# Optimization experiments

Hardware: AMD Instinct MI355X
Metric: run time of the kernel (lower is better)

## Reference

```python
import jax, jax.numpy as jnp
import numpy as np

DIM, E, K = 256, 8, 2
B, D, H, W = 1, 32, 32, 32
EPS = 1e-5


def setup_inputs() -> dict:
    key = jax.random.key(0)
    ks = jax.random.split(key, 16)
    nrm = lambda k, s, sc=0.02: jax.random.normal(k, s, jnp.float32) * sc
    def resblock_params(k):
        k1, k2, k3, k4 = jax.random.split(k, 4)
        return dict(
            c1w=nrm(k1, (DIM, DIM, 3, 3, 3)), c1b=jnp.zeros((DIM,), jnp.float32),
            g1=jax.random.uniform(k2, (DIM,), jnp.float32, 0.5, 1.5), be1=jnp.zeros((DIM,), jnp.float32),
            c2w=nrm(k3, (DIM, DIM, 3, 3, 3)), c2b=jnp.zeros((DIM,), jnp.float32),
            g2=jax.random.uniform(k4, (DIM,), jnp.float32, 0.5, 1.5), be2=jnp.zeros((DIM,), jnp.float32),
        )
    p1 = resblock_params(ks[5])
    p2 = resblock_params(ks[6])
    return {
        "x": jax.random.normal(ks[0], (B, DIM, D, H, W), jnp.float32),
        "wg": nrm(ks[1], (DIM, E)),
        "w1": nrm(ks[2], (E, DIM, DIM)), "b1": jnp.zeros((E, DIM), jnp.float32),
        "w2": nrm(ks[3], (E, DIM, DIM)), "b2": jnp.zeros((E, DIM), jnp.float32),
        "r1_c1w": p1["c1w"], "r1_c1b": p1["c1b"], "r1_g1": p1["g1"], "r1_be1": p1["be1"],
        "r1_c2w": p1["c2w"], "r1_c2b": p1["c2b"], "r1_g2": p1["g2"], "r1_be2": p1["be2"],
        "r2_c1w": p2["c1w"], "r2_c1b": p2["c1b"], "r2_g1": p2["g1"], "r2_be1": p2["be1"],
        "r2_c2w": p2["c2w"], "r2_c2b": p2["c2b"], "r2_g2": p2["g2"], "r2_be2": p2["be2"],
        "c8w": nrm(ks[4], (DIM, DIM, 1, 1, 1)), "c8b": jnp.zeros((DIM,), jnp.float32),
    }


def conv3d(x, w, b, pad):
    y = jax.lax.conv_general_dilated(
        x, w, window_strides=(1, 1, 1), padding=[(pad, pad)] * 3,
        dimension_numbers=("NCDHW", "OIDHW", "NCDHW"))
    return y + b[None, :, None, None, None]


def batchnorm(x, g, b):
    m = x.mean(axis=(0, 2, 3, 4), keepdims=True)
    v = x.var(axis=(0, 2, 3, 4), keepdims=True)
    return g[None, :, None, None, None] * (x - m) * jax.lax.rsqrt(v + EPS) + b[None, :, None, None, None]


def unet_res_block(x, c1w, c1b, g1, be1, c2w, c2b, g2, be2):
    out = jax.nn.leaky_relu(batchnorm(conv3d(x, c1w, c1b, 1), g1, be1), 0.01)
    out = batchnorm(conv3d(out, c2w, c2b, 1), g2, be2)
    return jax.nn.leaky_relu(out + x, 0.01)  # identity shortcut (in==out ch, stride 1)


def mom_block(x, wg, w1, b1, w2, b2):
    Bb, C, Dd, Hh, Ww = x.shape
    tokens = x.transpose(0, 2, 3, 4, 1).reshape(-1, C)  # [T, C]
    T = tokens.shape[0]
    probs = jax.nn.softmax(tokens @ wg, axis=-1)          # [T, E]
    vals, idx = jax.lax.top_k(probs, K)                   # [T, K]
    wts = vals / vals.sum(-1, keepdims=True)
    gates = jnp.zeros((T, E), probs.dtype).at[jnp.arange(T)[:, None], idx].set(wts)
    # dense expert MLPs (math-equivalent to gather/dispatch/combine)
    h = jax.nn.gelu(jnp.einsum("tc,ech->eth", tokens, w1) + b1[:, None, :])
    eo = jnp.einsum("eth,ehc->etc", h, w2) + b2[:, None, :]
    moe = jnp.einsum("te,etc->tc", gates, eo)             # [T, C]
    # switch-style load-balancing auxiliary loss
    density = (gates > 0).astype(probs.dtype).mean(0)     # fraction of tokens per expert
    density_proxy = probs.mean(0)
    aux = (density * density_proxy).sum() * E
    out = x + moe.reshape(Bb, Dd, Hh, Ww, C).transpose(0, 4, 1, 2, 3)
    return out, aux


def reference(x, wg, w1, b1, w2, b2,
              r1_c1w, r1_c1b, r1_g1, r1_be1, r1_c2w, r1_c2b, r1_g2, r1_be2,
              r2_c1w, r2_c1b, r2_g1, r2_be1, r2_c2w, r2_c2b, r2_g2, r2_be2,
              c8w, c8b):
    xm, aux = mom_block(x, wg, w1, b1, w2, b2)
    res = unet_res_block(xm, r1_c1w, r1_c1b, r1_g1, r1_be1, r1_c2w, r1_c2b, r1_g2, r1_be2)
    res = unet_res_block(res, r2_c1w, r2_c1b, r2_g1, r2_be1, r2_c2w, r2_c2b, r2_g2, r2_be2)
    out = xm + conv3d(res, c8w, c8b, 0)  # Dropout3d is identity at eval
    return out, aux
```

## Files before the change

kernel.cpp:

```cpp
#include <hip/hip_runtime.h>
#include <stdint.h>

typedef __attribute__((ext_vector_type(8))) short short8;
typedef __attribute__((ext_vector_type(4))) float f32x4;
typedef unsigned short u16;
typedef unsigned int u32;
typedef unsigned long long u64;

#define WS_TOK   0ull
#define WS_XT    16777216ull
#define WS_XMCT  50331648ull
#define WS_GATES 83886080ull
#define WS_H     84934656ull
#define WS_P1    135266304ull
#define WS_P2    155389952ull
#define WS_Y     175513600ull
#define WS_R2    209068032ull
#define WS_WRB   225845248ull
#define WS_W1P   240001024ull
#define WS_W2P   241049600ull
#define WS_C8P   242098176ull
#define WS_PART  242229248ull
#define WS_SF    243277824ull
#define WS_AUXP  243279872ull

#define WS_PERM  (WS_H + 0x00000ull)
#define WS_TBL   (WS_H + 0x60000ull)
#define WS_META  (WS_H + 0x70000ull)
#define WS_BCNT  (WS_H + 0x80000ull)
#define WS_BOFF  (WS_H + 0x90000ull)
#define WS_SEL   (WS_H + 0x100000ull)

__device__ __forceinline__ u16 f2bf(float f) {
  u32 x = __float_as_uint(f);
  u32 r = x + 0x7fffu + ((x >> 16) & 1u);
  return (u16)(r >> 16);
}
__device__ __forceinline__ float bf2f(u32 u) { return __uint_as_float(u << 16); }

__global__ void trans_in_k(const float* __restrict__ x, float* __restrict__ xt,
                           u16* __restrict__ tok) {
  __shared__ float ld[64][65];
  int tt = blockIdx.x, cc = blockIdx.y, tid = threadIdx.x;
#pragma unroll
  for (int k = 0; k < 16; ++k) {
    int idx = tid + k * 256;
    int cl = idx >> 6, j = idx & 63;
    ld[cl][j] = x[(size_t)(cc * 64 + cl) * 32768 + tt * 64 + j];
  }
  __syncthreads();
#pragma unroll
  for (int k = 0; k < 16; ++k) {
    int idx = tid + k * 256;
    int tl = idx >> 6, cl = idx & 63;
    float v = ld[cl][tl];
    size_t o = (size_t)(tt * 64 + tl) * 256 + cc * 64 + cl;
    xt[o] = v;
    tok[o] = f2bf(v);
  }
}

__global__ void pack_rb_k(const float* __restrict__ w0, const float* __restrict__ w1,
                          const float* __restrict__ w2, const float* __restrict__ w3,
                          u16* __restrict__ out) {
  __shared__ float ld[6912];
  int conv = blockIdx.x >> 8, blk = blockIdx.x & 255, tid = threadIdx.x;
  const float* src = conv == 0 ? w0 : conv == 1 ? w1 : conv == 2 ? w2 : w3;
  size_t base = (size_t)blk * 256 * 27;
#pragma unroll
  for (int k = 0; k < 27; ++k) ld[tid + k * 256] = src[base + tid + k * 256];
  __syncthreads();
  u16* dst = out + (size_t)conv * 27 * 65536;
  int n = blk * 256 + tid;
#pragma unroll
  for (int tap = 0; tap < 27; ++tap)
    dst[(size_t)tap * 65536 + n] = f2bf(ld[tid * 27 + tap]);
}

__global__ void pack_tr_k(const float* __restrict__ w1, const float* __restrict__ w2,
                          u16* __restrict__ w1p, u16* __restrict__ w2p) {
  __shared__ float ld[64][65];
  int m = blockIdx.y, tile = blockIdx.x, tid = threadIdx.x;
  const float* src = (m < 8) ? (w1 + (size_t)m * 65536) : (w2 + (size_t)(m - 8) * 65536);
  u16* dst = (m < 8) ? (w1p + (size_t)m * 65536) : (w2p + (size_t)(m - 8) * 65536);
  int r0 = (tile >> 2) * 64, c0 = (tile & 3) * 64;
#pragma unroll
  for (int k = 0; k < 16; ++k) {
    int idx = tid + k * 256;
    int rr = idx >> 6, cc = idx & 63;
    ld[rr][cc] = src[(size_t)(r0 + rr) * 256 + c0 + cc];
  }
  __syncthreads();
#pragma unroll
  for (int k = 0; k < 16; ++k) {
    int idx = tid + k * 256;
    int cc = idx >> 6, rr = idx & 63;
    dst[(size_t)(c0 + cc) * 256 + r0 + rr] = f2bf(ld[rr][cc]);
  }
}

__global__ void cvt_k(const float* __restrict__ in, u16* __restrict__ out, int n) {
  int i = blockIdx.x * 256 + threadIdx.x;
  if (i < n) out[i] = f2bf(in[i]);
}

__global__ void halo_k(u16* __restrict__ P1, u16* __restrict__ P2) {
  int gid = blockIdx.x * 256 + threadIdx.x;
  int r = gid >> 5, o = (gid & 31) << 3;
  if (r >= 39304) return;
  int d = r / 1156, rem = r - d * 1156, h = rem / 34, w = rem - h * 34;
  if (d >= 1 && d <= 32 && h >= 1 && h <= 32 && w >= 1 && w <= 32) return;
  uint4 z = {0u, 0u, 0u, 0u};
  *(uint4*)(P1 + (size_t)r * 256 + o) = z;
  *(uint4*)(P2 + (size_t)r * 256 + o) = z;
}

__global__ void gate_k(const float* __restrict__ x, const float* __restrict__ wg,
                       float* __restrict__ gw, u32* __restrict__ sel,
                       u32* __restrict__ blk_cnt, float* __restrict__ auxp) {
  __shared__ float wgs[2048];
  __shared__ float ax[4][16];
  __shared__ u32 bc[4][8];
  int tid = threadIdx.x;
#pragma unroll
  for (int k = 0; k < 8; ++k) wgs[tid + k * 256] = wg[tid + k * 256];
  __syncthreads();
  int t = blockIdx.x * 256 + tid;
  int lane = tid & 63, wv = tid >> 6;
  float l[8] = {0, 0, 0, 0, 0, 0, 0, 0};
#pragma unroll 4
  for (int c = 0; c < 256; ++c) {
    float xv = x[(size_t)c * 32768 + t];
#pragma unroll
    for (int e = 0; e < 8; ++e) l[e] += xv * wgs[c * 8 + e];
  }
  float mx = l[0];
#pragma unroll
  for (int e = 1; e < 8; ++e) mx = fmaxf(mx, l[e]);
  float p[8], sum = 0.f;
#pragma unroll
  for (int e = 0; e < 8; ++e) { p[e] = __expf(l[e] - mx); sum += p[e]; }
  float inv = 1.0f / sum;
#pragma unroll
  for (int e = 0; e < 8; ++e) p[e] *= inv;
  int i0 = 0; float v0 = p[0];
#pragma unroll
  for (int e = 1; e < 8; ++e) if (p[e] > v0) { v0 = p[e]; i0 = e; }
  int i1 = -1; float v1 = -1.0f;
#pragma unroll
  for (int e = 0; e < 8; ++e) if (e != i0 && p[e] > v1) { v1 = p[e]; i1 = e; }
  float wsum = v0 + v1;
  gw[t * 2] = v0 / wsum;
  gw[t * 2 + 1] = v1 / wsum;
  sel[t] = (u32)i0 | ((u32)i1 << 4);
  u64 mm[8];
#pragma unroll
  for (int e = 0; e < 8; ++e) mm[e] = __ballot(i0 == e || i1 == e);
  if (lane == 0) {
#pragma unroll
    for (int e = 0; e < 8; ++e) bc[wv][e] = (u32)__popcll(mm[e]);
  }
#pragma unroll
  for (int e = 0; e < 8; ++e) {
    float ps = p[e];
    float cn = (e == i0 || e == i1) ? 1.0f : 0.0f;
    for (int o = 32; o; o >>= 1) { ps += __shfl_down(ps, o); cn += __shfl_down(cn, o); }
    if (lane == 0) { ax[wv][e] = ps; ax[wv][8 + e] = cn; }
  }
  __syncthreads();
  if (tid < 16)
    auxp[blockIdx.x * 16 + tid] = ax[0][tid] + ax[1][tid] + ax[2][tid] + ax[3][tid];
  if (tid < 8)
    blk_cnt[blockIdx.x * 8 + tid] = bc[0][tid] + bc[1][tid] + bc[2][tid] + bc[3][tid];
}

__global__ void aux_k(const float* __restrict__ auxp, float* __restrict__ out) {
  __shared__ float s[16];
  int i = threadIdx.x;
  if (i < 16) {
    float a = 0;
    for (int b = 0; b < 128; ++b) a += auxp[b * 16 + i];
    s[i] = a;
  }
  __syncthreads();
  if (i == 0) {
    float r = 0;
    for (int e = 0; e < 8; ++e)
      r += (s[8 + e] * (1.0f / 32768.0f)) * (s[e] * (1.0f / 32768.0f));
    out[0] = r * 8.0f;
  }
}

__global__ void scan_k(const u32* __restrict__ blk_cnt, u32* __restrict__ blkoff,
                       u32* __restrict__ tbl, u32* __restrict__ meta,
                       u32* __restrict__ perm) {
  __shared__ u32 tot[8], base[8], nck[8], cbase[8];
  int tid = threadIdx.x;
  if (tid < 8) {
    u32 run = 0;
    for (int b = 0; b < 128; ++b) {
      blkoff[b * 8 + tid] = run;
      run += blk_cnt[b * 8 + tid];
    }
    tot[tid] = run;
  }
  __syncthreads();
  if (tid == 0) {
    u32 acc = 0, c = 0;
    for (int e = 0; e < 8; ++e) {
      base[e] = acc;
      u32 nc = (tot[e] + 127) >> 7;
      nck[e] = nc;
      cbase[e] = c;
      acc += nc << 7;
      c += nc;
    }
    meta[0] = c;
  }
  __syncthreads();
  for (int i = tid; i < 1024; i += 256) blkoff[i] += base[i & 7];
  if (tid < 8) {
    for (u32 k = 0; k < nck[tid]; ++k)
      tbl[cbase[tid] + k] = ((base[tid] + (k << 7)) << 4) | (u32)tid;
    for (u32 sl = base[tid] + tot[tid]; sl < base[tid] + (nck[tid] << 7); ++sl)
      perm[sl] = 0;
  }
}

__global__ void scatter_k(const u32* __restrict__ sel, const u32* __restrict__ blkoff,
                          u32* __restrict__ perm, u32* __restrict__ tpos) {
  __shared__ u32 wcnt[4][8];
  int tid = threadIdx.x, b = blockIdx.x;
  int lane = tid & 63, wv = tid >> 6;
  int t = b * 256 + tid;
  u32 s = sel[t];
  int i0 = s & 15, i1 = (s >> 4) & 15;
  u64 mm[8];
#pragma unroll
  for (int e = 0; e < 8; ++e) mm[e] = __ballot(i0 == e || i1 == e);
  if (lane == 0) {
#pragma unroll
    for (int e = 0; e < 8; ++e) wcnt[wv][e] = (u32)__popcll(mm[e]);
  }
  __syncthreads();
  u64 lt = (1ull << lane) - 1ull;
#pragma unroll
  for (int e = 0; e < 8; ++e) {
    bool is0 = (i0 == e), is1 = (i1 == e);
    if (is0 || is1) {
      u32 woff = 0;
#pragma unroll
      for (int w = 0; w < 4; ++w)
        if (w < wv) woff += wcnt[w][e];
      u32 pos = blkoff[b * 8 + e] + woff + (u32)__popcll(mm[e] & lt);
      perm[pos] = (u32)t;
      tpos[t * 2 + (is0 ? 0 : 1)] = pos;
    }
  }
}

__global__ __launch_bounds__(512, 2) void moe_gemm_k(
    const u16* __restrict__ tok, const u32* __restrict__ perm,
    const u32* __restrict__ tbl, const u32* __restrict__ meta,
    const u16* __restrict__ w1p, const u16* __restrict__ w2p,
    const float* __restrict__ b1, const float* __restrict__ b2,
    u16* __restrict__ eo) {
  __shared__ __attribute__((aligned(16))) unsigned char smem[163840];
  const int bid = blockIdx.x;
  if ((u32)bid >= meta[0]) return;
  const u32 ent = tbl[bid];
  const int e = (int)(ent & 15u);
  const int slot0 = (int)(ent >> 4);
  const int tid = threadIdx.x;
  const int lane = tid & 63;
  const int wv = tid >> 6;
  const int wr = (wv >> 2) * 64;
  const int wc = (wv & 3) * 64;
  const int fq = lane >> 4, fr = lane & 15;
  const u16* w1e = w1p + e * 65536;
  const u16* w2e = w2p + e * 65536;

#pragma unroll
  for (int it = 0; it < 8; ++it) {
    int s = tid + it * 512;
    int r = s >> 5, seg = s & 31;
    int cole = ((seg >> 3) << 6) + (((seg & 7) ^ (r & 7)) << 3);
    u32 rowtok = perm[slot0 + r];
    __builtin_amdgcn_global_load_lds(
        (const __attribute__((address_space(1))) u32*)(tok + (size_t)rowtok * 256 + cole),
        (__attribute__((address_space(3))) u32*)(smem + s * 16), 16, 0, 0);
  }

  f32x4 acc1[4][4];
#pragma unroll
  for (int mc = 0; mc < 4; ++mc)
#pragma unroll
    for (int nt = 0; nt < 4; ++nt) acc1[mc][nt] = (f32x4){0.f, 0.f, 0.f, 0.f};

#pragma unroll 1
  for (int kc = 0; kc < 4; ++kc) {
#pragma unroll
    for (int it = 0; it < 4; ++it) {
      int s = tid + it * 512;
      int r = s >> 3;
      int sub = (s & 7) ^ (r & 7);
      __builtin_amdgcn_global_load_lds(
          (const __attribute__((address_space(1))) u32*)(w1e + (size_t)r * 256 + kc * 64 + sub * 8),
          (__attribute__((address_space(3))) u32*)(smem + 65536 + s * 16), 16, 0, 0);
    }
    __syncthreads();
#pragma unroll
    for (int khf = 0; khf < 2; ++khf) {
      short8 af1[4], bt[4];
#pragma unroll
      for (int mc = 0; mc < 4; ++mc) {
        int row = wc + mc * 16 + fr;
        int p = (khf * 4 + fq) ^ (row & 7);
        af1[mc] = *(const short8*)(smem + 65536 + row * 128 + p * 16);
      }
#pragma unroll
      for (int nt = 0; nt < 4; ++nt) {
        int row = wr + nt * 16 + fr;
        int p = (khf * 4 + fq) ^ (row & 7);
        bt[nt] = *(const short8*)(smem + row * 512 + kc * 128 + p * 16);
      }
#pragma unroll
      for (int mc = 0; mc < 4; ++mc)
#pragma unroll
        for (int nt = 0; nt < 4; ++nt)
          acc1[mc][nt] = __builtin_amdgcn_mfma_f32_16x16x32_bf16(af1[mc], bt[nt], acc1[mc][nt], 0, 0, 0);
    }
    __syncthreads();
  }

#pragma unroll
  for (int mc = 0; mc < 4; ++mc) {
    int k0 = wc + mc * 16 + fq * 4;
    float4 bv = *(const float4*)(b1 + e * 256 + k0);
#pragma unroll
    for (int nt = 0; nt < 4; ++nt) {
      int t = wr + nt * 16 + fr;
      u64 pk = 0;
#pragma unroll
      for (int j = 0; j < 4; ++j) {
        float v = acc1[mc][nt][j] + ((const float*)&bv)[j];
        float u = 1.5957691216057308f * (v + 0.044715f * v * v * v);
        float g = v / (1.0f + __expf(-u));
        pk |= (u64)f2bf(g) << (16 * j);
      }
      *(u64*)(smem + 98304 + t * 512 + ((k0 * 2) ^ ((t & 7) << 4))) = pk;
    }
  }

  f32x4 acc2[4][4];
#pragma unroll
  for (int m = 0; m < 4; ++m)
#pragma unroll
    for (int n = 0; n < 4; ++n) acc2[m][n] = (f32x4){0.f, 0.f, 0.f, 0.f};

#pragma unroll 1
  for (int kc = 0; kc < 4; ++kc) {
#pragma unroll
    for (int it = 0; it < 4; ++it) {
      int s = tid + it * 512;
      int r = s >> 3;
      int sub = (s & 7) ^ (r & 7);
      __builtin_amdgcn_global_load_lds(
          (const __attribute__((address_space(1))) u32*)(w2e + (size_t)r * 256 + kc * 64 + sub * 8),
          (__attribute__((address_space(3))) u32*)(smem + 65536 + s * 16), 16, 0, 0);
    }
    __syncthreads();
#pragma unroll
    for (int khf = 0; khf < 2; ++khf) {
      short8 af[4], bb[4];
#pragma unroll
      for (int m = 0; m < 4; ++m) {
        int row = wr + m * 16 + fr;
        int col = (kc * 128 + (khf * 4 + fq) * 16) ^ ((row & 7) << 4);
        af[m] = *(const short8*)(smem + 98304 + row * 512 + col);
      }
#pragma unroll
      for (int n = 0; n < 4; ++n) {
        int row = wc + n * 16 + fr;
        int p = (khf * 4 + fq) ^ (row & 7);
        bb[n] = *(const short8*)(smem + 65536 + row * 128 + p * 16);
      }
#pragma unroll
      for (int m = 0; m < 4; ++m)
#pragma unroll
        for (int n = 0; n < 4; ++n)
          acc2[m][n] = __builtin_amdgcn_mfma_f32_16x16x32_bf16(af[m], bb[n], acc2[m][n], 0, 0, 0);
    }
    __syncthreads();
  }

  float bs2[4];
#pragma unroll
  for (int n = 0; n < 4; ++n) bs2[n] = b2[e * 256 + wc + n * 16 + fr];
#pragma unroll
  for (int m = 0; m < 4; ++m)
#pragma unroll
    for (int j = 0; j < 4; ++j) {
      int rowslot = slot0 + wr + m * 16 + fq * 4 + j;
      u16* er = eo + (size_t)rowslot * 256 + wc;
#pragma unroll
      for (int n = 0; n < 4; ++n) er[n * 16 + fr] = f2bf(acc2[m][n][j] + bs2[n]);
    }
}

__global__ void combine_k(float* __restrict__ xt, const u16* __restrict__ eo,
                          const float* __restrict__ gw, const u32* __restrict__ tpos,
                          float* __restrict__ xmct, u16* __restrict__ pad) {
  __shared__ float ld[64][65];
  __shared__ u32 pp[64][2];
  __shared__ float gg[64][2];
  int tt = blockIdx.x, cc = blockIdx.y, tid = threadIdx.x;
  if (tid < 128) {
    int tl = tid >> 1, s = tid & 1;
    int t = tt * 64 + tl;
    pp[tl][s] = tpos[t * 2 + s];
    gg[tl][s] = gw[t * 2 + s];
  }
  __syncthreads();
#pragma unroll
  for (int k = 0; k < 16; ++k) {
    int idx = tid + k * 256;
    int tl = idx >> 6, cl = idx & 63;
    int c = cc * 64 + cl;
    size_t o = (size_t)(tt * 64 + tl) * 256 + c;
    float e0 = bf2f(eo[(size_t)pp[tl][0] * 256 + c]);
    float e1 = bf2f(eo[(size_t)pp[tl][1] * 256 + c]);
    float v = xt[o] + gg[tl][0] * e0 + gg[tl][1] * e1;
    xt[o] = v;
    ld[tl][cl] = v;
    int t = tt * 64 + tl;
    int d = t >> 10, h = (t >> 5) & 31, w = t & 31;
    int prow = (d + 1) * 1156 + (h + 1) * 34 + (w + 1);
    pad[(size_t)prow * 256 + c] = f2bf(v);
  }
  __syncthreads();
#pragma unroll
  for (int k = 0; k < 16; ++k) {
    int idx = tid + k * 256;
    int cl = idx >> 6, tl = idx & 63;
    xmct[(size_t)(cc * 64 + cl) * 32768 + tt * 64 + tl] = ld[tl][cl];
  }
}

template <int MODE>
__global__ __launch_bounds__(256, 2) void gemm_k(
    const u16* __restrict__ A, const u16* __restrict__ Bw,
    const float* __restrict__ bias, u16* __restrict__ yB,
    float* __restrict__ outF, const float* __restrict__ xmct,
    float* __restrict__ part) {
  __shared__ __attribute__((aligned(16))) unsigned char smem[65536];
  const int tid = threadIdx.x;
  const int bx = blockIdx.x;
  const int ttile = (MODE == 0) ? ((bx & 7) * 32 + (bx >> 3)) : bx;
  const int ctile = blockIdx.y;
  const int lane = tid & 63;
  const int wv = tid >> 6;
  const int wr = (wv >> 1) << 6;
  const int wc = (wv & 1) << 6;
  const int fq = lane >> 4;
  const int fr = lane & 15;

  int aoff[4], boff[4];
#pragma unroll
  for (int it = 0; it < 4; ++it) {
    int s = tid + it * 256;
    int r = s >> 3;
    int lsg = (s & 7) ^ (r & 7);
    if (MODE == 0) {
      int dd = ttile >> 3;
      int h0 = (ttile & 7) << 2;
      int base = dd * 1156 + (h0 + (r >> 5)) * 34 + (r & 31);
      aoff[it] = base * 256 + lsg * 8;
    } else {
      aoff[it] = (ttile * 128 + r) * 256 + lsg * 8;
    }
    boff[it] = (ctile * 128 + r) * 256 + lsg * 8;
  }

  f32x4 acc[4][4];
#pragma unroll
  for (int m = 0; m < 4; ++m)
#pragma unroll
    for (int n = 0; n < 4; ++n) acc[m][n] = (f32x4){0.f, 0.f, 0.f, 0.f};

  const int nStep = (MODE == 0) ? 108 : 4;

  auto stage = [&](int s, int buf) {
    int tap = (MODE == 0) ? (s >> 2) : 0;
    int kc = s & 3;
    int atap = 0, btap = 0;
    if (MODE == 0) {
      atap = ((tap / 9) * 1156 + ((tap / 3) % 3) * 34 + (tap % 3)) * 256;
      btap = tap * 65536;
    }
    const u16* Ak = A + atap + kc * 64;
    const u16* Bk = Bw + btap + kc * 64;
    unsigned char* sb = smem + buf * 32768;
#pragma unroll
    for (int it = 0; it < 4; ++it) {
      __builtin_amdgcn_global_load_lds(
          (const __attribute__((address_space(1))) u32*)(Ak + aoff[it]),
          (__attribute__((address_space(3))) u32*)(sb + (tid + it * 256) * 16),
          16, 0, 0);
      __builtin_amdgcn_global_load_lds(
          (const __attribute__((address_space(1))) u32*)(Bk + boff[it]),
          (__attribute__((address_space(3))) u32*)(sb + 16384 + (tid + it * 256) * 16),
          16, 0, 0);
    }
  };

  auto compute = [&](int buf) {
    unsigned char* sb = smem + buf * 32768;
#pragma unroll
    for (int khf = 0; khf < 2; ++khf) {
      short8 af[4], bb[4];
#pragma unroll
      for (int m = 0; m < 4; ++m) {
        int row = wr + m * 16 + fr;
        int p = (khf * 4 + fq) ^ (row & 7);
        af[m] = *(const short8*)(sb + row * 128 + p * 16);
      }
#pragma unroll
      for (int n = 0; n < 4; ++n) {
        int row = wc + n * 16 + fr;
        int p = (khf * 4 + fq) ^ (row & 7);
        bb[n] = *(const short8*)(sb + 16384 + row * 128 + p * 16);
      }
#pragma unroll
      for (int m = 0; m < 4; ++m)
#pragma unroll
        for (int n = 0; n < 4; ++n)
          acc[m][n] = __builtin_amdgcn_mfma_f32_16x16x32_bf16(af[m], bb[n], acc[m][n], 0, 0, 0);
    }
  };

  stage(0, 0);
  asm volatile("s_waitcnt vmcnt(0)" ::: "memory");
  __builtin_amdgcn_s_barrier();
  int cur = 0;
#pragma unroll 1
  for (int s = 0; s < nStep; ++s) {
    if (s + 1 < nStep) stage(s + 1, cur ^ 1);
    compute(cur);
    asm volatile("s_waitcnt vmcnt(0)" ::: "memory");
    __builtin_amdgcn_s_barrier();
    cur ^= 1;
  }

  float bs[4];
#pragma unroll
  for (int n = 0; n < 4; ++n) bs[n] = bias[ctile * 128 + wc + n * 16 + fr];

  if (MODE == 3) {
#pragma unroll
    for (int m = 0; m < 4; ++m) {
      int trow = ttile * 128 + wr + m * 16 + fq * 4;
#pragma unroll
      for (int n = 0; n < 4; ++n) {
        int oc = ctile * 128 + wc + n * 16 + fr;
        size_t o = (size_t)oc * 32768 + trow;
        float4 xv = *(const float4*)(xmct + o);
        float4 w;
        w.x = acc[m][n][0] + bs[n] + xv.x;
        w.y = acc[m][n][1] + bs[n] + xv.y;
        w.z = acc[m][n][2] + bs[n] + xv.z;
        w.w = acc[m][n][3] + bs[n] + xv.w;
        *(float4*)(outF + o) = w;
      }
    }
  } else {
    float sn[4] = {0, 0, 0, 0}, qn[4] = {0, 0, 0, 0};
#pragma unroll
    for (int m = 0; m < 4; ++m) {
#pragma unroll
      for (int j = 0; j < 4; ++j) {
        int t = ttile * 128 + wr + m * 16 + fq * 4 + j;
        u16* yr = yB + (size_t)t * 256 + ctile * 128 + wc;
#pragma unroll
        for (int n = 0; n < 4; ++n) {
          float v = acc[m][n][j] + bs[n];
          yr[n * 16 + fr] = f2bf(v);
          sn[n] += v;
          qn[n] += v * v;
        }
      }
    }
#pragma unroll
    for (int n = 0; n < 4; ++n) {
      float s = sn[n], q = qn[n];
      s += __shfl_xor(s, 16); s += __shfl_xor(s, 32);
      q += __shfl_xor(q, 16); q += __shfl_xor(q, 32);
      if (lane < 16) {
        int pi = (ttile * 2 + (wv >> 1)) * 256 + ctile * 128 + wc + n * 16 + fr;
        part[pi] = s;
        part[131072 + pi] = q;
      }
    }
  }
}

__global__ void stats2_k(const float* __restrict__ part, const float* __restrict__ g,
                         const float* __restrict__ be, float* __restrict__ sf) {
  __shared__ float sred[16][16], qred[16][16];
  int tid = threadIdx.x;
  int cl = tid & 15, ch = tid >> 4;
  int c = blockIdx.x * 16 + cl;
  float s = 0, q = 0;
  for (int b = ch * 32; b < ch * 32 + 32; ++b) {
    s += part[b * 256 + c];
    q += part[131072 + b * 256 + c];
  }
  sred[ch][cl] = s;
  qred[ch][cl] = q;
  __syncthreads();
  if (ch == 0) {
    s = 0; q = 0;
#pragma unroll
    for (int k = 0; k < 16; ++k) { s += sred[k][cl]; q += qred[k][cl]; }
    float mean = s * (1.0f / 32768.0f);
    float var = q * (1.0f / 32768.0f) - mean * mean;
    float a = g[c] * rsqrtf(var + 1e-5f);
    sf[c] = a;
    sf[256 + c] = be[c] - mean * a;
  }
}

template <int V>
__global__ void bn_k(const u16* __restrict__ y, const float* __restrict__ sf,
                     const float* __restrict__ skip, u16* __restrict__ pad,
                     float* __restrict__ f32o, u16* __restrict__ bfo) {
  int gid = blockIdx.x * 256 + threadIdx.x;
  int t = gid >> 5, c0 = (gid & 31) << 3;
  size_t base = (size_t)t * 256 + c0;
  float v[8];
  uint4 yv = *(const uint4*)(y + base);
  v[0] = bf2f(yv.x & 0xffffu); v[1] = bf2f(yv.x >> 16);
  v[2] = bf2f(yv.y & 0xffffu); v[3] = bf2f(yv.y >> 16);
  v[4] = bf2f(yv.z & 0xffffu); v[5] = bf2f(yv.z >> 16);
  v[6] = bf2f(yv.w & 0xffffu); v[7] = bf2f(yv.w >> 16);
  const float4* ap = (const float4*)(sf + c0);
  float4 a0 = ap[0], a1 = ap[1];
  const float4* shp = (const float4*)(sf + 256 + c0);
  float4 s0 = shp[0], s1 = shp[1];
  v[0] = a0.x * v[0] + s0.x; v[1] = a0.y * v[1] + s0.y;
  v[2] = a0.z * v[2] + s0.z; v[3] = a0.w * v[3] + s0.w;
  v[4] = a1.x * v[4] + s1.x; v[5] = a1.y * v[5] + s1.y;
  v[6] = a1.z * v[6] + s1.z; v[7] = a1.w * v[7] + s1.w;
  if (V >= 1) {
    const float4* kp = (const float4*)(skip + base);
    float4 k0 = kp[0], k1 = kp[1];
    v[0] += k0.x; v[1] += k0.y; v[2] += k0.z; v[3] += k0.w;
    v[4] += k1.x; v[5] += k1.y; v[6] += k1.z; v[7] += k1.w;
  }
#pragma unroll
  for (int i = 0; i < 8; ++i) v[i] = v[i] > 0.0f ? v[i] : 0.01f * v[i];
  if (V <= 1) {
    int d = t >> 10, h = (t >> 5) & 31, w = t & 31;
    int prow = (d + 1) * 1156 + (h + 1) * 34 + (w + 1);
    uint4 pk;
    pk.x = (u32)f2bf(v[0]) | ((u32)f2bf(v[1]) << 16);
    pk.y = (u32)f2bf(v[2]) | ((u32)f2bf(v[3]) << 16);
    pk.z = (u32)f2bf(v[4]) | ((u32)f2bf(v[5]) << 16);
    pk.w = (u32)f2bf(v[6]) | ((u32)f2bf(v[7]) << 16);
    *(uint4*)(pad + (size_t)prow * 256 + c0) = pk;
  }
  if (V == 1) {
    float4 o0 = {v[0], v[1], v[2], v[3]}, o1 = {v[4], v[5], v[6], v[7]};
    float4* fp = (float4*)(f32o + base);
    fp[0] = o0; fp[1] = o1;
  }
  if (V == 2) {
    uint4 pk;
    pk.x = (u32)f2bf(v[0]) | ((u32)f2bf(v[1]) << 16);
    pk.y = (u32)f2bf(v[2]) | ((u32)f2bf(v[3]) << 16);
    pk.z = (u32)f2bf(v[4]) | ((u32)f2bf(v[5]) << 16);
    pk.w = (u32)f2bf(v[6]) | ((u32)f2bf(v[7]) << 16);
    *(uint4*)(bfo + base) = pk;
  }
}

extern "C" void kernel_launch(void* const* d_in, const int* in_sizes, int n_in,
                              void* d_out, int out_size, void* d_ws, size_t ws_size,
                              hipStream_t stream) {
  (void)in_sizes; (void)n_in; (void)out_size; (void)ws_size;
  const float* x  = (const float*)d_in[0];
  const float* wg = (const float*)d_in[1];
  const float* w1 = (const float*)d_in[2];
  const float* b1 = (const float*)d_in[3];
  const float* w2 = (const float*)d_in[4];
  const float* b2 = (const float*)d_in[5];

  char* ws = (char*)d_ws;
  u16* tok    = (u16*)(ws + WS_TOK);
  float* xt   = (float*)(ws + WS_XT);
  float* xmct = (float*)(ws + WS_XMCT);
  float* gw   = (float*)(ws + WS_GATES);
  u32* tpos   = (u32*)(ws + WS_GATES + 0x80000ull);
  u32* perm   = (u32*)(ws + WS_PERM);
  u32* tbl    = (u32*)(ws + WS_TBL);
  u32* meta   = (u32*)(ws + WS_META);
  u32* bcnt   = (u32*)(ws + WS_BCNT);
  u32* boff   = (u32*)(ws + WS_BOFF);
  u32* selb   = (u32*)(ws + WS_SEL);
  u16* P1     = (u16*)(ws + WS_P1);
  u16* P2     = (u16*)(ws + WS_P2);
  u16* ybuf   = (u16*)(ws + WS_Y);
  u16* eo     = (u16*)(ws + WS_Y);
  u16* r2b    = (u16*)(ws + WS_R2);
  u16* wrb    = (u16*)(ws + WS_WRB);
  u16* w1p    = (u16*)(ws + WS_W1P);
  u16* w2p    = (u16*)(ws + WS_W2P);
  u16* c8p    = (u16*)(ws + WS_C8P);
  float* part = (float*)(ws + WS_PART);
  float* sf   = (float*)(ws + WS_SF);
  float* auxp = (float*)(ws + WS_AUXP);
  float* outp = (float*)d_out;

  halo_k<<<4913, 256, 0, stream>>>(P1, P2);
  gate_k<<<128, 256, 0, stream>>>(x, wg, gw, selb, bcnt, auxp);
  trans_in_k<<<dim3(512, 4), 256, 0, stream>>>(x, xt, tok);
  pack_rb_k<<<1024, 256, 0, stream>>>((const float*)d_in[6], (const float*)d_in[10],
                                      (const float*)d_in[14], (const float*)d_in[18], wrb);
  pack_tr_k<<<dim3(16, 16), 256, 0, stream>>>(w1, w2, w1p, w2p);
  cvt_k<<<256, 256, 0, stream>>>((const float*)d_in[22], c8p, 65536);

  scan_k<<<1, 256, 0, stream>>>(bcnt, boff, tbl, meta, perm);
  scatter_k<<<128, 256, 0, stream>>>(selb, boff, perm, tpos);
  moe_gemm_k<<<520, 512, 0, stream>>>(tok, perm, tbl, meta, w1p, w2p, b1, b2, eo);
  combine_k<<<dim3(512, 4), 256, 0, stream>>>(xt, eo, gw, tpos, xmct, P1);

  gemm_k<0><<<dim3(256, 2), 256, 0, stream>>>(P1, wrb + 0 * 1769472, (const float*)d_in[7],
                                              ybuf, nullptr, nullptr, part);
  stats2_k<<<16, 256, 0, stream>>>(part, (const float*)d_in[8], (const float*)d_in[9], sf);
  bn_k<0><<<4096, 256, 0, stream>>>(ybuf, sf, nullptr, P2, nullptr, nullptr);
  gemm_k<0><<<dim3(256, 2), 256, 0, stream>>>(P2, wrb + 1 * 1769472, (const float*)d_in[11],
                                              ybuf, nullptr, nullptr, part);
  stats2_k<<<16, 256, 0, stream>>>(part, (const float*)d_in[12], (const float*)d_in[13], sf);
  bn_k<1><<<4096, 256, 0, stream>>>(ybuf, sf, xt, P1, xt, nullptr);

  gemm_k<0><<<dim3(256, 2), 256, 0, stream>>>(P1, wrb + 2 * 1769472, (const float*)d_in[15],
                                              ybuf, nullptr, nullptr, part);
  stats2_k<<<16, 256, 0, stream>>>(part, (const float*)d_in[16], (const float*)d_in[17], sf);
  bn_k<0><<<4096, 256, 0, stream>>>(ybuf, sf, nullptr, P2, nullptr, nullptr);
  gemm_k<0><<<dim3(256, 2), 256, 0, stream>>>(P2, wrb + 3 * 1769472, (const float*)d_in[19],
                                              ybuf, nullptr, nullptr, part);
  stats2_k<<<16, 256, 0, stream>>>(part, (const float*)d_in[20], (const float*)d_in[21], sf);
  bn_k<2><<<4096, 256, 0, stream>>>(ybuf, sf, xt, nullptr, nullptr, r2b);

  gemm_k<3><<<dim3(256, 2), 256, 0, stream>>>(r2b, c8p, (const float*)d_in[23], nullptr,
                                              outp, xmct, nullptr);
  aux_k<<<1, 64, 0, stream>>>(auxp, outp + 8388608);
}
```

Measured before the change: 675.8 us.

## Double-buffer expert weight tiles in MoE GEMM and reuse token LDS for hidden

The MoE expert GEMM kernel now prefetches the next 64-wide weight chunk into an alternate LDS buffer while the current chunk is being consumed. The last W1 iteration already prefetches the first W2 chunk, and the per-thread weight offsets are hoisted out of the loops. The GELU hidden tile now overwrites the token tile region, which shrinks LDS from 160KB to 128KB. The aim is to hide weight-load latency behind MFMA work. The risk is that buffer reuse depends on the existing barriers at the end of each iteration.

```diff
diff --git a/kernel.cpp b/kernel.cpp
--- a/kernel.cpp
+++ b/kernel.cpp
@@ -265,7 +265,7 @@
     const u16* __restrict__ w1p, const u16* __restrict__ w2p,
     const float* __restrict__ b1, const float* __restrict__ b2,
     u16* __restrict__ eo) {
-  __shared__ __attribute__((aligned(16))) unsigned char smem[163840];
+  __shared__ __attribute__((aligned(16))) unsigned char smem[131072];
   const int bid = blockIdx.x;
   if ((u32)bid >= meta[0]) return;
   const u32 ent = tbl[bid];
@@ -280,6 +280,14 @@
   const u16* w1e = w1p + e * 65536;
   const u16* w2e = w2p + e * 65536;
 
+  int woff[4];
+#pragma unroll
+  for (int it = 0; it < 4; ++it) {
+    int s = tid + it * 512;
+    int r = s >> 3;
+    woff[it] = r * 256 + (((s & 7) ^ (r & 7)) << 3);
+  }
+
 #pragma unroll
   for (int it = 0; it < 8; ++it) {
     int s = tid + it * 512;
@@ -290,6 +298,13 @@
         (const __attribute__((address_space(1))) u32*)(tok + (size_t)rowtok * 256 + cole),
         (__attribute__((address_space(3))) u32*)(smem + s * 16), 16, 0, 0);
   }
+#pragma unroll
+  for (int it = 0; it < 4; ++it)
+    __builtin_amdgcn_global_load_lds(
+        (const __attribute__((address_space(1))) u32*)(w1e + woff[it]),
+        (__attribute__((address_space(3))) u32*)(smem + 65536 + (tid + it * 512) * 16),
+        16, 0, 0);
+  __syncthreads();
 
   f32x4 acc1[4][4];
 #pragma unroll
@@ -299,16 +314,15 @@
 
 #pragma unroll 1
   for (int kc = 0; kc < 4; ++kc) {
-#pragma unroll
-    for (int it = 0; it < 4; ++it) {
-      int s = tid + it * 512;
-      int r = s >> 3;
-      int sub = (s & 7) ^ (r & 7);
+    const u16* nw = (kc < 3) ? (w1e + (kc + 1) * 64) : w2e;
+    unsigned char* nb = smem + 65536 + (((kc + 1) & 1) * 32768);
+#pragma unroll
+    for (int it = 0; it < 4; ++it)
       __builtin_amdgcn_global_load_lds(
-          (const __attribute__((address_space(1))) u32*)(w1e + (size_t)r * 256 + kc * 64 + sub * 8),
-          (__attribute__((address_space(3))) u32*)(smem + 65536 + s * 16), 16, 0, 0);
-    }
-    __syncthreads();
+          (const __attribute__((address_space(1))) u32*)(nw + woff[it]),
+          (__attribute__((address_space(3))) u32*)(nb + (tid + it * 512) * 16),
+          16, 0, 0);
+    const unsigned char* wb = smem + 65536 + ((kc & 1) * 32768);
 #pragma unroll
     for (int khf = 0; khf < 2; ++khf) {
       short8 af1[4], bt[4];
@@ -316,7 +330,7 @@
       for (int mc = 0; mc < 4; ++mc) {
         int row = wc + mc * 16 + fr;
         int p = (khf * 4 + fq) ^ (row & 7);
-        af1[mc] = *(const short8*)(smem + 65536 + row * 128 + p * 16);
+        af1[mc] = *(const short8*)(wb + row * 128 + p * 16);
       }
 #pragma unroll
       for (int nt = 0; nt < 4; ++nt) {
@@ -348,9 +362,10 @@
         float g = v / (1.0f + __expf(-u));
         pk |= (u64)f2bf(g) << (16 * j);
       }
-      *(u64*)(smem + 98304 + t * 512 + ((k0 * 2) ^ ((t & 7) << 4))) = pk;
-    }
-  }
+      *(u64*)(smem + t * 512 + ((k0 * 2) ^ ((t & 7) << 4))) = pk;
+    }
+  }
+  __syncthreads();
 
   f32x4 acc2[4][4];
 #pragma unroll
@@ -360,16 +375,17 @@
 
 #pragma unroll 1
   for (int kc = 0; kc < 4; ++kc) {
-#pragma unroll
-    for (int it = 0; it < 4; ++it) {
-      int s = tid + it * 512;
-      int r = s >> 3;
-      int sub = (s & 7) ^ (r & 7);
-      __builtin_amdgcn_global_load_lds(
-          (const __attribute__((address_space(1))) u32*)(w2e + (size_t)r * 256 + kc * 64 + sub * 8),
-          (__attribute__((address_space(3))) u32*)(smem + 65536 + s * 16), 16, 0, 0);
-    }
-    __syncthreads();
+    if (kc < 3) {
+      unsigned char* nb = smem + 65536 + (((kc + 1) & 1) * 32768);
+      const u16* nw = w2e + (kc + 1) * 64;
+#pragma unroll
+      for (int it = 0; it < 4; ++it)
+        __builtin_amdgcn_global_load_lds(
+            (const __attribute__((address_space(1))) u32*)(nw + woff[it]),
+            (__attribute__((address_space(3))) u32*)(nb + (tid + it * 512) * 16),
+            16, 0, 0);
+    }
+    const unsigned char* wb = smem + 65536 + ((kc & 1) * 32768);
 #pragma unroll
     for (int khf = 0; khf < 2; ++khf) {
       short8 af[4], bb[4];
@@ -377,13 +393,13 @@
       for (int m = 0; m < 4; ++m) {
         int row = wr + m * 16 + fr;
         int col = (kc * 128 + (khf * 4 + fq) * 16) ^ ((row & 7) << 4);
-        af[m] = *(const short8*)(smem + 98304 + row * 512 + col);
+        af[m] = *(const short8*)(smem + row * 512 + col);
       }
 #pragma unroll
       for (int n = 0; n < 4; ++n) {
         int row = wc + n * 16 + fr;
         int p = (khf * 4 + fq) ^ (row & 7);
-        bb[n] = *(const short8*)(smem + 65536 + row * 128 + p * 16);
+        bb[n] = *(const short8*)(wb + row * 128 + p * 16);
       }
 #pragma unroll
       for (int m = 0; m < 4; ++m)
@@ -515,7 +531,7 @@
   };
 
   auto compute = [&](int buf) {
-    unsigned char* sb = smem + buf * 32768;
+    const unsigned char* sb = smem + buf * 32768;
 #pragma unroll
     for (int khf = 0; khf < 2; ++khf) {
       short8 af[4], bb[4];
```

Result: no change. 670.4 us (-0.8%).
